# Kernel optimization log

Hardware: AMD Instinct MI355X
Metric: run time of the kernel (lower is better)

## Reference

```python
import jax, jax.numpy as jnp
import numpy as np

B, L, T = 2048, 4096, 2


def setup_inputs() -> dict:
    key = jax.random.key(0)
    k1, k2, k3, k4, k5 = jax.random.split(key, 5)
    emissions = jax.random.normal(k1, (B, L, T), dtype=jnp.float32)
    # params initialized uniform(-0.1, 0.1) as in the torch module
    transitions = jax.random.uniform(k2, (T, T), minval=-0.1, maxval=0.1, dtype=jnp.float32)
    start_transitions = jax.random.uniform(k3, (T,), minval=-0.1, maxval=0.1, dtype=jnp.float32)
    end_transitions = jax.random.uniform(k4, (T,), minval=-0.1, maxval=0.1, dtype=jnp.float32)
    tags = jax.random.randint(k5, (B, L), 0, T).astype(jnp.int64)
    mask = jnp.ones((B, L), dtype=bool)
    return {"emissions": emissions, "transitions": transitions,
            "start_transitions": start_transitions, "end_transitions": end_transitions,
            "tags": tags, "mask": mask}


def _gold_score(emissions, transitions, start_transitions, end_transitions, tags, mask):
    # score of the given tag path; transitions[to, from]
    score = start_transitions[tags[:, 0]] \
        + jnp.take_along_axis(emissions[:, 0], tags[:, 0:1], axis=1)[:, 0]
    emit = jnp.take_along_axis(emissions[:, 1:], tags[:, 1:, None], axis=2)[..., 0]  # [B, L-1]
    trans = transitions[tags[:, 1:], tags[:, :-1]]                                   # [B, L-1]
    score = score + jnp.sum((emit + trans) * mask[:, 1:].astype(emit.dtype), axis=1)
    last_idx = jnp.sum(mask, axis=1).astype(jnp.int32) - 1
    last_tags = jnp.take_along_axis(tags, last_idx[:, None].astype(tags.dtype), axis=1)[:, 0]
    return score + end_transitions[last_tags]


def _normalizer(emissions, transitions, start_transitions, end_transitions, mask):
    # forward algorithm in log space via lax.scan over time
    alpha0 = start_transitions + emissions[:, 0]  # [B, T]

    def step(alpha, inp):
        emit, m = inp  # emit: [B, T], m: [B]
        scores = alpha[:, None, :] + transitions[None, :, :]  # [B, to, from]
        alpha_new = jax.nn.logsumexp(scores, axis=2) + emit
        alpha = jnp.where(m[:, None], alpha_new, alpha)
        return alpha, None

    emit_t = jnp.swapaxes(emissions[:, 1:], 0, 1)  # [L-1, B, T]
    mask_t = jnp.swapaxes(mask[:, 1:], 0, 1)       # [L-1, B]
    alpha, _ = jax.lax.scan(step, alpha0, (emit_t, mask_t))
    return jax.nn.logsumexp(alpha + end_transitions, axis=1)


def reference(emissions, transitions, start_transitions, end_transitions, tags, mask):
    """CRF NLL loss (reduction='mean'), per-token normalized, as in CRFLayer._compute_loss."""
    gold = _gold_score(emissions, transitions, start_transitions, end_transitions, tags, mask)
    logZ = _normalizer(emissions, transitions, start_transitions, end_transitions, mask)
    seq_lengths = jnp.clip(jnp.sum(mask, axis=1).astype(emissions.dtype), 1.0)
    nll = (logZ - gold) / seq_lengths
    return jnp.mean(nll)
```

## Files before the change

kernel.cpp:

```cpp
#include <hip/hip_runtime.h>
#include <math.h>

#define LSEQ  4096
#define BATCH 2048
#define CHUNK 16
#define BLOCK 256
#define LOG2E 1.4426950408889634f
#define LN2   0.6931471805599453f

__device__ __forceinline__ float exp2_fast(float x) {
    float r; asm("v_exp_f32 %0, %1" : "=v"(r) : "v"(x)); return r;
}
__device__ __forceinline__ float log2_fast(float x) {
    float r; asm("v_log_f32 %0, %1" : "=v"(r) : "v"(x)); return r;
}
__device__ __forceinline__ float lse2b(float a, float b) {
    float m = fmaxf(a, b);
    float d = fminf(a, b) - m;
    return m + log2_fast(1.0f + exp2_fast(d));
}

__global__ __launch_bounds__(BLOCK) void crf_row_kernel(
    const float* __restrict__ emis,
    const float* __restrict__ trans,
    const float* __restrict__ startt,
    const float* __restrict__ endt,
    const int*   __restrict__ tags,
    float*       __restrict__ nll_out)
{
    const int b    = blockIdx.x;
    const int tid  = threadIdx.x;
    const int lane = tid & 63;
    const int wave = tid >> 6;
    const int t0   = tid * CHUNK;

    const float t00 = trans[0], t01 = trans[1], t10 = trans[2], t11 = trans[3];
    const float s0 = startt[0], s1 = startt[1];
    const float P00 = exp2_fast(t00 * LOG2E), P01 = exp2_fast(t01 * LOG2E);
    const float P10 = exp2_fast(t10 * LOG2E), P11 = exp2_fast(t11 * LOG2E);

    const float4* erow = reinterpret_cast<const float4*>(emis + ((size_t)b * LSEQ + t0) * 2);
    float e0[CHUNK], e1[CHUNK];
    #pragma unroll
    for (int i = 0; i < 8; ++i) {
        float4 v = erow[i];
        e0[2*i]   = v.x; e1[2*i]   = v.y;
        e0[2*i+1] = v.z; e1[2*i+1] = v.w;
    }

    const int4* trow = reinterpret_cast<const int4*>(tags + (size_t)b * LSEQ + t0);
    int tg[CHUNK];
    #pragma unroll
    for (int i = 0; i < 4; ++i) {
        int4 v = trow[i];
        tg[4*i] = v.x; tg[4*i+1] = v.y; tg[4*i+2] = v.z; tg[4*i+3] = v.w;
    }
    const int pidx = (tid == 0) ? 0 : (t0 - 1);
    const int prev = tags[(size_t)b * LSEQ + pidx];

    float g = 0.0f;
    int c11, ccur, cprev; float Pf;
    if (tid == 0) {
        g = tg[0] ? s1 : s0;
        c11 = 0; ccur = 0; cprev = 0; Pf = 15.0f;
    } else {
        c11 = tg[0] & prev; ccur = tg[0]; cprev = prev; Pf = 16.0f;
    }
    g += tg[0] ? e1[0] : e0[0];
    int p = tg[0];
    #pragma unroll
    for (int i = 1; i < CHUNK; ++i) {
        g    += tg[i] ? e1[i] : e0[i];
        c11  += tg[i] & p;
        ccur += tg[i];
        cprev += p;
        p = tg[i];
    }
    if (tid == BLOCK - 1) g += tg[CHUNK-1] ? endt[1] : endt[0];
    {
        float f11 = (float)c11, fc = (float)ccur, fp = (float)cprev;
        g += t11 * f11 + t10 * (fc - f11) + t01 * (fp - f11)
           + t00 * (Pf - fc - fp + f11);
    }

    float a0, a1, b0c, b1c;
    {
        float E0 = exp2_fast(e0[0] * LOG2E);
        float E1 = exp2_fast(e1[0] * LOG2E);
        if (tid == 0) {
            a0 = exp2_fast((s0 + e0[0]) * LOG2E);
            a1 = exp2_fast((s1 + e1[0]) * LOG2E);
            b0c = a0; b1c = a1;
        } else {
            a0  = P00 * E0; a1  = P10 * E1;
            b0c = P01 * E0; b1c = P11 * E1;
        }
    }
    #pragma unroll
    for (int i = 1; i < CHUNK; ++i) {
        float F0 = exp2_fast(e0[i] * LOG2E);
        float F1 = exp2_fast(e1[i] * LOG2E);
        float na0 = F0 * fmaf(P00, a0,  P01 * a1);
        float na1 = F1 * fmaf(P10, a0,  P11 * a1);
        float nb0 = F0 * fmaf(P00, b0c, P01 * b1c);
        float nb1 = F1 * fmaf(P10, b0c, P11 * b1c);
        a0 = na0; a1 = na1; b0c = nb0; b1c = nb1;
    }

    float lc0  = log2_fast(a0);
    float lc1  = log2_fast(a1);
    float beta = log2_fast(b0c) - lc0;

    #pragma unroll
    for (int s = 1; s < 64; s <<= 1) {
        float plc0 = __shfl_down(lc0,  s, 64);
        float plc1 = __shfl_down(lc1,  s, 64);
        float pb   = __shfl_down(beta, s, 64);
        float pg   = __shfl_down(g,    s, 64);
        float sv = lse2b(lc0, lc1 + pb);
        lc0 = plc0 + sv;
        lc1 = plc1 + sv;
        g  += pg;
    }

    __shared__ float sR[4][4];
    if (lane == 0) {
        sR[wave][0] = lc0; sR[wave][1] = lc1; sR[wave][2] = beta; sR[wave][3] = g;
    }
    __syncthreads();
    if (tid == 0) {
        float c0 = sR[0][0], c1 = sR[0][1], gg = sR[0][3];
        #pragma unroll
        for (int w = 1; w < 4; ++w) {
            float sv = lse2b(c0, c1 + sR[w][2]);
            c0 = sR[w][0] + sv;
            c1 = sR[w][1] + sv;
            gg += sR[w][3];
        }
        float logZ = lse2b(c0 + endt[0] * LOG2E, c1 + endt[1] * LOG2E) * LN2;
        nll_out[b] = (logZ - gg) * (1.0f / (float)LSEQ);
    }
}

__global__ __launch_bounds__(256) void mean_kernel(
    const float* __restrict__ nll, float* __restrict__ out)
{
    int tid = threadIdx.x;
    const float4* v = reinterpret_cast<const float4*>(nll);
    float4 a = v[tid], b = v[tid + 256];
    float acc = ((a.x + a.y) + (a.z + a.w)) + ((b.x + b.y) + (b.z + b.w));
    #pragma unroll
    for (int s = 1; s < 64; s <<= 1) acc += __shfl_down(acc, s, 64);
    __shared__ float sw[4];
    if ((tid & 63) == 0) sw[tid >> 6] = acc;
    __syncthreads();
    if (tid == 0) out[0] = ((sw[0] + sw[1]) + (sw[2] + sw[3])) * (1.0f / (float)BATCH);
}

extern "C" void kernel_launch(void* const* d_in, const int* in_sizes, int n_in,
                              void* d_out, int out_size, void* d_ws, size_t ws_size,
                              hipStream_t stream) {
    const float* emis   = (const float*)d_in[0];
    const float* trans  = (const float*)d_in[1];
    const float* startt = (const float*)d_in[2];
    const float* endt   = (const float*)d_in[3];
    const int*   tags   = (const int*)d_in[4];

    float* nll = (float*)d_ws;
    float* out = (float*)d_out;

    crf_row_kernel<<<BATCH, BLOCK, 0, stream>>>(emis, trans, startt, endt, tags, nll);
    mean_kernel<<<1, 256, 0, stream>>>(nll, out);
}
```

Baseline: 23.81 us.

## Split each CRF row across two blocks with coalesced LDS-staged loads

Each sequence row is now handled by two blocks, each covering half the sequence with 8 steps per thread, so the grid doubles to 4096 blocks. Emissions are loaded with fully coalesced float4 reads and staged through XOR-swizzled shared memory, so the gold-score pass and the forward-scan pass each read them in their own layout. Each half-block writes its partial log-space transfer state, and the finish kernel merges the two halves, adds the end transitions and takes the mean. The aim is better memory coalescing and more parallelism, at the cost of an extra LDS round trip, a barrier and a heavier single-block finish kernel.

```diff
diff --git a/kernel.cpp b/kernel.cpp
--- a/kernel.cpp
+++ b/kernel.cpp
@@ -2,9 +2,10 @@
 #include <math.h>
 
 #define LSEQ  4096
+#define HALF  2048
 #define BATCH 2048
-#define CHUNK 16
 #define BLOCK 256
+#define CHUNK 8
 #define LOG2E 1.4426950408889634f
 #define LN2   0.6931471805599453f
 
@@ -19,75 +20,95 @@
     float d = fminf(a, b) - m;
     return m + log2_fast(1.0f + exp2_fast(d));
 }
-
-__global__ __launch_bounds__(BLOCK) void crf_row_kernel(
+__device__ __forceinline__ int SW(int h) { return h ^ ((h >> 3) & 7); }
+
+__global__ __launch_bounds__(BLOCK) void crf_half_kernel(
     const float* __restrict__ emis,
     const float* __restrict__ trans,
     const float* __restrict__ startt,
     const float* __restrict__ endt,
     const int*   __restrict__ tags,
-    float*       __restrict__ nll_out)
+    float4*      __restrict__ out4)
 {
-    const int b    = blockIdx.x;
-    const int tid  = threadIdx.x;
-    const int lane = tid & 63;
-    const int wave = tid >> 6;
-    const int t0   = tid * CHUNK;
+    const int Bid  = blockIdx.x;
+    const int row  = Bid >> 1, half = Bid & 1;
+    const int T    = threadIdx.x;
+    const int lane = T & 63, wave = T >> 6;
+
+    const size_t ebase = ((size_t)row * LSEQ + (size_t)half * HALF) * 2;
+    const size_t tbase = (size_t)row * LSEQ + (size_t)half * HALF;
+    const float4* eg4 = reinterpret_cast<const float4*>(emis + ebase);
+    const int4*   tg4 = reinterpret_cast<const int4*>(tags + tbase);
+
+    __shared__ float4 lds[1024];
+    __shared__ float  sR[4][4];
 
     const float t00 = trans[0], t01 = trans[1], t10 = trans[2], t11 = trans[3];
+    const float T00 = t00 * LOG2E, T01 = t01 * LOG2E, T10 = t10 * LOG2E, T11 = t11 * LOG2E;
+    const float P00 = exp2_fast(T00), P01 = exp2_fast(T01);
+    const float P10 = exp2_fast(T10), P11 = exp2_fast(T11);
     const float s0 = startt[0], s1 = startt[1];
-    const float P00 = exp2_fast(t00 * LOG2E), P01 = exp2_fast(t01 * LOG2E);
-    const float P10 = exp2_fast(t10 * LOG2E), P11 = exp2_fast(t11 * LOG2E);
-
-    const float4* erow = reinterpret_cast<const float4*>(emis + ((size_t)b * LSEQ + t0) * 2);
-    float e0[CHUNK], e1[CHUNK];
-    #pragma unroll
-    for (int i = 0; i < 8; ++i) {
-        float4 v = erow[i];
-        e0[2*i]   = v.x; e1[2*i]   = v.y;
-        e0[2*i+1] = v.z; e1[2*i+1] = v.w;
-    }
-
-    const int4* trow = reinterpret_cast<const int4*>(tags + (size_t)b * LSEQ + t0);
-    int tg[CHUNK];
-    #pragma unroll
-    for (int i = 0; i < 4; ++i) {
-        int4 v = trow[i];
-        tg[4*i] = v.x; tg[4*i+1] = v.y; tg[4*i+2] = v.z; tg[4*i+3] = v.w;
-    }
-    const int pidx = (tid == 0) ? 0 : (t0 - 1);
-    const int prev = tags[(size_t)b * LSEQ + pidx];
+
+    float4 st[4];
+    #pragma unroll
+    for (int j = 0; j < 4; ++j) st[j] = eg4[T + 256 * j];
+    int4 tgv0 = tg4[T];
+    int4 tgv1 = tg4[T + 256];
+    int prev0 = 0, prev1 = 0;
+    if (lane == 0) {
+        int f0 = T, f1 = T + 256;
+        prev0 = (half == 0 && f0 == 0) ? 0 : tags[tbase + 4 * (size_t)f0 - 1];
+        prev1 = tags[tbase + 4 * (size_t)f1 - 1];
+    }
+    #pragma unroll
+    for (int j = 0; j < 4; ++j) lds[SW(T + 256 * j)] = st[j];
+    __syncthreads();
 
     float g = 0.0f;
-    int c11, ccur, cprev; float Pf;
-    if (tid == 0) {
-        g = tg[0] ? s1 : s0;
-        c11 = 0; ccur = 0; cprev = 0; Pf = 15.0f;
-    } else {
-        c11 = tg[0] & prev; ccur = tg[0]; cprev = prev; Pf = 16.0f;
-    }
-    g += tg[0] ? e1[0] : e0[0];
-    int p = tg[0];
-    #pragma unroll
-    for (int i = 1; i < CHUNK; ++i) {
-        g    += tg[i] ? e1[i] : e0[i];
-        c11  += tg[i] & p;
-        ccur += tg[i];
-        cprev += p;
-        p = tg[i];
-    }
-    if (tid == BLOCK - 1) g += tg[CHUNK-1] ? endt[1] : endt[0];
+    int c11 = 0, ccur = 0, cprev = 0;
+    const bool ownsStart = (half == 0) && (T == 0);
+    #pragma unroll
+    for (int i = 0; i < 2; ++i) {
+        int  f  = T + 256 * i;
+        int4 tv = (i == 0) ? tgv0 : tgv1;
+        float4 E0 = lds[SW(2 * f)];
+        float4 E1 = lds[SW(2 * f + 1)];
+        g += (tv.x ? E0.y : E0.x);
+        g += (tv.y ? E0.w : E0.z);
+        g += (tv.z ? E1.y : E1.x);
+        g += (tv.w ? E1.w : E1.z);
+        int pt = __shfl_up(tv.w, 1, 64);
+        if (lane == 0) pt = (i == 0) ? prev0 : prev1;
+        bool isStart = ownsStart && (i == 0);
+        if (!isStart) { c11 += pt & tv.x; ccur += tv.x; cprev += pt; }
+        else          { g += (tv.x ? s1 : s0); }
+        c11 += tv.x & tv.y;  ccur += tv.y;  cprev += tv.x;
+        c11 += tv.y & tv.z;  ccur += tv.z;  cprev += tv.y;
+        c11 += tv.z & tv.w;  ccur += tv.w;  cprev += tv.z;
+    }
+    if (half == 1 && T == BLOCK - 1) g += (tgv1.w ? endt[1] : endt[0]);
     {
         float f11 = (float)c11, fc = (float)ccur, fp = (float)cprev;
+        float Pf = ownsStart ? 7.0f : 8.0f;
         g += t11 * f11 + t10 * (fc - f11) + t01 * (fp - f11)
            + t00 * (Pf - fc - fp + f11);
+    }
+
+    float4 S[4];
+    #pragma unroll
+    for (int j = 0; j < 4; ++j) S[j] = lds[SW(4 * T + j)];
+    float e0[CHUNK], e1[CHUNK];
+    #pragma unroll
+    for (int j = 0; j < 4; ++j) {
+        e0[2*j]   = S[j].x; e1[2*j]   = S[j].y;
+        e0[2*j+1] = S[j].z; e1[2*j+1] = S[j].w;
     }
 
     float a0, a1, b0c, b1c;
     {
         float E0 = exp2_fast(e0[0] * LOG2E);
         float E1 = exp2_fast(e1[0] * LOG2E);
-        if (tid == 0) {
+        if (ownsStart) {
             a0 = exp2_fast((s0 + e0[0]) * LOG2E);
             a1 = exp2_fast((s1 + e1[0]) * LOG2E);
             b0c = a0; b1c = a1;
@@ -123,12 +144,11 @@
         g  += pg;
     }
 
-    __shared__ float sR[4][4];
     if (lane == 0) {
         sR[wave][0] = lc0; sR[wave][1] = lc1; sR[wave][2] = beta; sR[wave][3] = g;
     }
     __syncthreads();
-    if (tid == 0) {
+    if (T == 0) {
         float c0 = sR[0][0], c1 = sR[0][1], gg = sR[0][3];
         #pragma unroll
         for (int w = 1; w < 4; ++w) {
@@ -137,18 +157,28 @@
             c1 = sR[w][1] + sv;
             gg += sR[w][3];
         }
-        float logZ = lse2b(c0 + endt[0] * LOG2E, c1 + endt[1] * LOG2E) * LN2;
-        nll_out[b] = (logZ - gg) * (1.0f / (float)LSEQ);
-    }
-}
-
-__global__ __launch_bounds__(256) void mean_kernel(
-    const float* __restrict__ nll, float* __restrict__ out)
+        out4[Bid] = make_float4(c0, c1, beta, gg);
+    }
+}
+
+__global__ __launch_bounds__(256) void finish_kernel(
+    const float4* __restrict__ h4,
+    const float*  __restrict__ endt,
+    float*        __restrict__ out)
 {
-    int tid = threadIdx.x;
-    const float4* v = reinterpret_cast<const float4*>(nll);
-    float4 a = v[tid], b = v[tid + 256];
-    float acc = ((a.x + a.y) + (a.z + a.w)) + ((b.x + b.y) + (b.z + b.w));
+    const int tid = threadIdx.x;
+    const float e0 = endt[0] * LOG2E, e1 = endt[1] * LOG2E;
+    float acc = 0.0f;
+    #pragma unroll
+    for (int r8 = 0; r8 < BATCH / 256; ++r8) {
+        int row = tid + 256 * r8;
+        float4 A  = h4[2 * row];
+        float4 Bv = h4[2 * row + 1];
+        float sv = lse2b(A.x, A.y + Bv.z);
+        float c0 = Bv.x + sv, c1 = Bv.y + sv;
+        float logZ = lse2b(c0 + e0, c1 + e1) * LN2;
+        acc += (logZ - (A.w + Bv.w)) * (1.0f / (float)LSEQ);
+    }
     #pragma unroll
     for (int s = 1; s < 64; s <<= 1) acc += __shfl_down(acc, s, 64);
     __shared__ float sw[4];
@@ -166,9 +196,9 @@
     const float* endt   = (const float*)d_in[3];
     const int*   tags   = (const int*)d_in[4];
 
-    float* nll = (float*)d_ws;
-    float* out = (float*)d_out;
-
-    crf_row_kernel<<<BATCH, BLOCK, 0, stream>>>(emis, trans, startt, endt, tags, nll);
-    mean_kernel<<<1, 256, 0, stream>>>(nll, out);
-}
+    float4* reps = (float4*)d_ws;
+    float*  out  = (float*)d_out;
+
+    crf_half_kernel<<<2 * BATCH, BLOCK, 0, stream>>>(emis, trans, startt, endt, tags, reps);
+    finish_kernel<<<1, 256, 0, stream>>>(reps, endt, out);
+}
```

Result: slower. 24.90 us (+4.6%).
